# Performance work log

Hardware: AMD Instinct MI355X
Metric: run time of the kernel (lower is better)

Reference implementation:

```python
import jax, jax.numpy as jnp
import numpy as np

B, C, H, W, K = 4, 32, 64, 64, 64
BH, BW = 2, 2  # block_size
RF_THRESH = 0.05  # gaussian support threshold (lattice kernels are ~0 outside RF)


def _gaussian_lattice(key, n_kernels, h, w):
    """Build Gaussian receptive-field kernels like lattice.gaussian_kernel_lattice:
    rfs[k,i,j] = exp(-((i-mu_y)^2 + (j-mu_x)^2) / (2*sigma^2)), thresholded to
    zero outside the RF so each kernel has compact support."""
    k1, k2 = jax.random.split(key)
    mu = jax.random.uniform(k1, (n_kernels, 2), minval=8.0, maxval=h - 8.0)
    sigma = jax.random.uniform(k2, (n_kernels, 1), minval=4.0, maxval=7.0)
    yy = jnp.arange(h, dtype=jnp.float32)[:, None]
    xx = jnp.arange(w, dtype=jnp.float32)[None, :]
    d2 = (yy[None] - mu[:, 0, None, None]) ** 2 + (xx[None] - mu[:, 1, None, None]) ** 2
    g = jnp.exp(-d2 / (2.0 * sigma[:, :, None] ** 2))  # (K, h, w)
    return jnp.where(g > RF_THRESH, g, 0.0).astype(jnp.float32)


def setup_inputs() -> dict:
    key = jax.random.key(0)
    ku, kr = jax.random.split(key)
    u = jax.random.normal(ku, (B, C, H, W), dtype=jnp.float32)
    rfs = _gaussian_lattice(kr, K, H, W)
    return {"u": u, "rfs": rfs}


def reference(u, rfs):
    """RF_Pool.__call__ with pool_type='prob', block_size=(2,2): returns p_mean.

    For each receptive field k, the kernel is elementwise-multiplied with u and
    a probabilistic max-pool (Lee et al.) with an 'off' state is computed over
    the RF support:  h_mean_k = exp(u*rf_k) / (1 + sum_{RF_k} exp(u*rf_k)).
    Detection probabilities are accumulated over RFs, then pooling-unit means
    p_mean are taken as the block-wise max over block_size blocks."""
    dt = u.dtype
    mask = rfs > 0  # (K, H, W) RF supports
    neg = jnp.asarray(-1e30, dt)
    # kernel-weighted pre-activations per RF: (B, C, K, H, W)
    v = u[:, :, None, :, :] * rfs[None, None]
    vm = jnp.where(mask[None, None], v, neg)
    # stable normalization including the off-state exp(0)=1
    m = jnp.maximum(jnp.max(vm, axis=(-2, -1), keepdims=True), 0.0)
    e = jnp.where(mask[None, None], jnp.exp(v - m), 0.0)
    denom = jnp.exp(-m) + jnp.sum(e, axis=(-2, -1), keepdims=True)
    h_mean = jnp.sum(e / denom, axis=2)  # (B, C, H, W) sum over RFs
    # block-wise pooling to p_mean: (B, C, H//BH, W//BW)
    p_mean = h_mean.reshape(B, C, H // BH, BH, W // BW, BW).max(axis=(3, 5))
    return p_mean
```

## Files before the change

kernel.cpp:

```cpp
#include <hip/hip_runtime.h>
#include <hip/hip_bf16.h>

#define BB 4
#define CC 32
#define HH 64
#define WW 64
#define KK 64
#define PIX (HH * WW)
#define NBC (BB * CC)


__global__ __launch_bounds__(256) void rf_phase1(
        const float* __restrict__ u,
        const float* __restrict__ rfs,
        float* __restrict__ inv) {
    const int bc = blockIdx.x >> 4;
    const int kg = blockIdx.x & 15;
    const int t = threadIdx.x, w = t >> 6, l = t & 63;

    __shared__ float su[PIX];
    {
        const float4* u4  = (const float4*)(u + (size_t)bc * PIX);
        float4*       su4 = (float4*)su;
        #pragma unroll
        for (int i = 0; i < 4; ++i) su4[t + 256 * i] = u4[t + 256 * i];
    }
    __syncthreads();

    const int k = kg * 4 + w;
    const float4* r4  = (const float4*)(rfs + (size_t)k * PIX);
    const float4* su4 = (const float4*)su;

    float s = 0.f;
    #pragma unroll
    for (int i = 0; i < 16; ++i) {
        const float4 rv = r4[i * 64 + l];
        const float4 uv = su4[i * 64 + l];
        s += (rv.x > 0.f) ? __expf(uv.x * rv.x) : 0.f;
        s += (rv.y > 0.f) ? __expf(uv.y * rv.y) : 0.f;
        s += (rv.z > 0.f) ? __expf(uv.z * rv.z) : 0.f;
        s += (rv.w > 0.f) ? __expf(uv.w * rv.w) : 0.f;
    }
    #pragma unroll
    for (int off = 32; off > 0; off >>= 1)
        s += __shfl_xor(s, off, 64);
    if (l == 0) inv[bc * KK + k] = 1.f / (1.f + s);
}

__global__ __launch_bounds__(256) void rf_phase2(
        const float* __restrict__ u,
        const float* __restrict__ rfs,
        const float* __restrict__ inv,
        float* __restrict__ out) {
    const int rp  = blockIdx.x >> 5;
    const int bcq = blockIdx.x & 31;
    const int t = threadIdx.x, w = t >> 6, l = t & 63;
    const int r0 = rp * 2;
    const int bc = bcq * 4 + w;

    __shared__ float srf[2][KK][WW];
    __shared__ float sinv[256];

    #pragma unroll
    for (int i = 0; i < 8; ++i) {
        const int idx = i * 256 + t;
        const int k = idx >> 5, sub = idx & 31;
        const int row = sub >> 4, c4 = sub & 15;
        *(float4*)&srf[row][k][c4 * 4] =
            *(const float4*)(rfs + (size_t)k * PIX + (r0 + row) * WW + c4 * 4);
    }
    sinv[t] = inv[bcq * 256 + t];

    const float u0 = u[(size_t)bc * PIX + r0 * WW + l];
    const float u1 = u[(size_t)bc * PIX + r0 * WW + WW + l];
    __syncthreads();

    float h0 = 0.f, h1 = 0.f;
    #pragma unroll 16
    for (int k = 0; k < KK; ++k) {
        const float rv0 = srf[0][k][l];
        const float rv1 = srf[1][k][l];
        const float fi  = sinv[w * 64 + k];
        h0 += (rv0 > 0.f) ? __expf(u0 * rv0) * fi : 0.f;
        h1 += (rv1 > 0.f) ? __expf(u1 * rv1) * fi : 0.f;
    }

    const float v = fmaxf(h0, h1);
    const float o = fmaxf(v, __shfl_xor(v, 1, 64));
    if ((l & 1) == 0)
        out[(size_t)bc * (HH / 2) * (WW / 2) + rp * 32 + (l >> 1)] = o;
}

extern "C" void kernel_launch(void* const* d_in, const int* in_sizes, int n_in,
                              void* d_out, int out_size, void* d_ws, size_t ws_size,
                              hipStream_t stream) {
    const float* u   = (const float*)d_in[0];
    const float* rfs = (const float*)d_in[1];
    float* out       = (float*)d_out;
    float* inv       = (float*)d_ws;

    rf_phase1<<<NBC * 16, 256, 0, stream>>>(u, rfs, inv);
    rf_phase2<<<32 * 32, 256, 0, stream>>>(u, rfs, inv, out);
}
```

Measured before the change: 79.08 us.

## Read RF weights directly from global memory in phase2 and remap threads to pool pairs

```diff
diff --git a/kernel.cpp b/kernel.cpp
--- a/kernel.cpp
+++ b/kernel.cpp
@@ -47,48 +47,36 @@
     if (l == 0) inv[bc * KK + k] = 1.f / (1.f + s);
 }
 
-__global__ __launch_bounds__(256) void rf_phase2(
+__global__ __launch_bounds__(256, 4) void rf_phase2(
         const float* __restrict__ u,
         const float* __restrict__ rfs,
         const float* __restrict__ inv,
         float* __restrict__ out) {
-    const int rp  = blockIdx.x >> 5;
-    const int bcq = blockIdx.x & 31;
-    const int t = threadIdx.x, w = t >> 6, l = t & 63;
-    const int r0 = rp * 2;
-    const int bc = bcq * 4 + w;
+    const int bc = blockIdx.x >> 3;
+    const int rp = (blockIdx.x & 7) * 4 + (threadIdx.x >> 6);
+    const int l  = threadIdx.x & 63;
 
-    __shared__ float srf[2][KK][WW];
-    __shared__ float sinv[256];
+    const int row  = rp * 2 + (l >> 5);
+    const int col2 = (l & 31) * 2;
+    const size_t poff = (size_t)row * WW + col2;
 
-    #pragma unroll
-    for (int i = 0; i < 8; ++i) {
-        const int idx = i * 256 + t;
-        const int k = idx >> 5, sub = idx & 31;
-        const int row = sub >> 4, c4 = sub & 15;
-        *(float4*)&srf[row][k][c4 * 4] =
-            *(const float4*)(rfs + (size_t)k * PIX + (r0 + row) * WW + c4 * 4);
-    }
-    sinv[t] = inv[bcq * 256 + t];
-
-    const float u0 = u[(size_t)bc * PIX + r0 * WW + l];
-    const float u1 = u[(size_t)bc * PIX + r0 * WW + WW + l];
-    __syncthreads();
+    const float2 uv = *(const float2*)(u + (size_t)bc * PIX + poff);
+    const float* __restrict__ invp = inv + bc * KK;
+    const float* __restrict__ rfp  = rfs + poff;
 
     float h0 = 0.f, h1 = 0.f;
     #pragma unroll 16
     for (int k = 0; k < KK; ++k) {
-        const float rv0 = srf[0][k][l];
-        const float rv1 = srf[1][k][l];
-        const float fi  = sinv[w * 64 + k];
-        h0 += (rv0 > 0.f) ? __expf(u0 * rv0) * fi : 0.f;
-        h1 += (rv1 > 0.f) ? __expf(u1 * rv1) * fi : 0.f;
+        const float2 rv = *(const float2*)(rfp + (size_t)k * PIX);
+        const float fi  = invp[k];
+        h0 += (rv.x > 0.f) ? __expf(uv.x * rv.x) * fi : 0.f;
+        h1 += (rv.y > 0.f) ? __expf(uv.y * rv.y) * fi : 0.f;
     }
 
-    const float v = fmaxf(h0, h1);
-    const float o = fmaxf(v, __shfl_xor(v, 1, 64));
-    if ((l & 1) == 0)
-        out[(size_t)bc * (HH / 2) * (WW / 2) + rp * 32 + (l >> 1)] = o;
+    const float hm = fmaxf(h0, h1);
+    const float o  = fmaxf(hm, __shfl_xor(hm, 32, 64));
+    if (l < 32)
+        out[(size_t)bc * (HH / 2) * (WW / 2) + rp * 32 + l] = o;
 }
 
 extern "C" void kernel_launch(void* const* d_in, const int* in_sizes, int n_in,
@@ -100,5 +88,5 @@
     float* inv       = (float*)d_ws;
 
     rf_phase1<<<NBC * 16, 256, 0, stream>>>(u, rfs, inv);
-    rf_phase2<<<32 * 32, 256, 0, stream>>>(u, rfs, inv, out);
+    rf_phase2<<<NBC * 8, 256, 0, stream>>>(u, rfs, inv, out);
 }
```

Result: no change. 79.06 us (-0.0%).
